# Performance work log

Measured on AMD Instinct MI355X. Metric: run time of the kernel, lower is better.

## Reference

```python
import jax, jax.numpy as jnp
import numpy as np

B, C, W, H = 2, 64, 96, 96
C8 = C // 8


def setup_inputs() -> dict:
    key = jax.random.key(0)
    ks = jax.random.split(key, 8)
    return {
        "x": jax.random.normal(ks[0], (B, C, W, H), dtype=jnp.float32),
        "Wq": jax.random.normal(ks[1], (C8, C), dtype=jnp.float32) * 0.05,
        "bq": jax.random.normal(ks[2], (C8,), dtype=jnp.float32) * 0.05,
        "Wk": jax.random.normal(ks[3], (C8, C), dtype=jnp.float32) * 0.05,
        "bk": jax.random.normal(ks[4], (C8,), dtype=jnp.float32) * 0.05,
        "Wv": jax.random.normal(ks[5], (C, C), dtype=jnp.float32) * 0.05,
        "bv": jax.random.normal(ks[6], (C,), dtype=jnp.float32) * 0.05,
        "gamma": jax.random.normal(ks[7], (1,), dtype=jnp.float32),
    }


def reference(x, Wq, bq, Wk, bk, Wv, bv, gamma):
    b, c, w, h = x.shape
    n = w * h
    xf = x.reshape(b, c, n)  # [B, C, N]
    # 1x1 convs are channel-mixing matmuls over flattened spatial dim
    q = jnp.einsum('oc,bcn->bno', Wq, xf) + bq          # [B, N, C//8] (proj_query, permuted)
    k = jnp.einsum('oc,bcn->bon', Wk, xf) + bk[:, None]  # [B, C//8, N] (proj_key)
    energy = jnp.einsum('bno,bom->bnm', q, k)            # [B, N, N]
    # torch softmax over dim=1 (the query index), NOT the usual dim=-1
    attn = jax.nn.softmax(energy, axis=1)                # [B, N, N]
    v = jnp.einsum('oc,bcn->bon', Wv, xf) + bv[:, None]  # [B, C, N]
    # bmm(V, attn.permute(0,2,1)): out[b,c,m] = sum_n V[b,c,n] * attn[b,m,n]
    out = jnp.einsum('bcn,bmn->bcm', v, attn).reshape(b, c, w, h)
    return gamma * out + x
```

## Files before the change

kernel.cpp:

```cpp
#include <hip/hip_runtime.h>
#include <math.h>

#define NN 9216
#define LOG2E 1.4426950408889634f

typedef __attribute__((ext_vector_type(8))) __bf16 bf16x8;
typedef __attribute__((ext_vector_type(16))) float f32x16;
typedef __attribute__((ext_vector_type(4))) unsigned int u32x4;

#define MFMA32(a,b,c) __builtin_amdgcn_mfma_f32_32x32x16_bf16(a,b,c,0,0,0)

#if __has_builtin(__builtin_amdgcn_exp2f)
#define EXP2(x) __builtin_amdgcn_exp2f(x)
#else
#define EXP2(x) exp2f(x)
#endif

__device__ __forceinline__ bf16x8 zero8() {
    bf16x8 z;
    #pragma unroll
    for (int i = 0; i < 8; i++) z[i] = (__bf16)0.0f;
    return z;
}

__device__ __forceinline__ unsigned int pk2(float a, float b) {
    unsigned short ua = __builtin_bit_cast(unsigned short, (__bf16)a);
    unsigned short ub = __builtin_bit_cast(unsigned short, (__bf16)b);
    return (unsigned int)ua | ((unsigned int)ub << 16);
}

__device__ __forceinline__ void plane_swap(unsigned int &a, unsigned int &b) {
    asm("v_permlane32_swap_b32 %0, %1" : "+v"(a), "+v"(b));
}

__device__ __forceinline__ void cp16(void* lds, const void* g) {
    __builtin_amdgcn_global_load_lds(
        (const __attribute__((address_space(1))) unsigned int*)g,
        (__attribute__((address_space(3))) unsigned int*)lds, 16, 0, 0);
}

#define OFF_QB 0
#define OFF_KB 294912
#define OFF_VB 589824
#define OFF_DP 2949120
#define OFF_PARTS 2949120
#define WS_NEED 21823488ULL

__global__ __launch_bounds__(256) void qkv_kernel(
    const float* __restrict__ x,
    const float* __restrict__ Wq, const float* __restrict__ bq,
    const float* __restrict__ Wk, const float* __restrict__ bk,
    const float* __restrict__ Wv, const float* __restrict__ bv,
    __bf16* __restrict__ QB, __bf16* __restrict__ KB, __bf16* __restrict__ VB)
{
    __shared__ float wvs[1024], wqs[512], wks[512], bvs[16], bqs[8], bks[8];
    int tid = threadIdx.x;
    int z = blockIdx.z, b = blockIdx.y;
    for (int i = tid; i < 1024; i += 256) wvs[i] = Wv[z*1024 + i];
    if (z == 0)
        for (int i = tid; i < 512; i += 256) { wqs[i] = Wq[i]; wks[i] = Wk[i]; }
    if (tid < 16) bvs[tid] = bv[z*16 + tid];
    if (tid < 8)  { bqs[tid] = bq[tid]; bks[tid] = bk[tid]; }
    __syncthreads();

    int n = blockIdx.x * 256 + tid;

    float xc[64];
    #pragma unroll
    for (int c = 0; c < 64; c++) xc[c] = x[((size_t)(b*64 + c))*NN + n];

    float v[16];
    #pragma unroll
    for (int o = 0; o < 16; o++) v[o] = bvs[o];
    #pragma unroll
    for (int c = 0; c < 64; c++) {
        float xv = xc[c];
        #pragma unroll
        for (int o = 0; o < 16; o++) v[o] = fmaf(wvs[o*64+c], xv, v[o]);
    }
    #pragma unroll
    for (int o = 0; o < 16; o++)
        VB[((size_t)(b*64 + z*16 + o))*NN + n] = (__bf16)v[o];

    if (z == 0) {
        float q[8], k[8];
        #pragma unroll
        for (int o = 0; o < 8; o++) { q[o] = bqs[o]; k[o] = bks[o]; }
        #pragma unroll
        for (int c = 0; c < 64; c++) {
            float xv = xc[c];
            #pragma unroll
            for (int o = 0; o < 8; o++) {
                q[o] = fmaf(wqs[o*64+c], xv, q[o]);
                k[o] = fmaf(wks[o*64+c], xv, k[o]);
            }
        }
        bf16x8 qv, kv;
        #pragma unroll
        for (int o = 0; o < 8; o++) {
            qv[o] = (__bf16)(q[o] * LOG2E);
            kv[o] = (__bf16)k[o];
        }
        *(bf16x8*)(QB + ((size_t)b*NN + n)*8) = qv;
        *(bf16x8*)(KB + ((size_t)b*NN + n)*8) = kv;
    }
}

__global__ __launch_bounds__(256) void stats_kernel(
    const __bf16* __restrict__ QB, const __bf16* __restrict__ KB,
    float* __restrict__ Dp)
{
    __shared__ float Dl[4][32];
    int tid = threadIdx.x;
    int lane = tid & 63, w = tid >> 6;
    int l31 = lane & 31, h = lane >> 5;
    int b = blockIdx.y, z = blockIdx.z;
    int n0 = blockIdx.x * 32;

    f32x16 Z16;
    #pragma unroll
    for (int r = 0; r < 16; r++) Z16[r] = 0.0f;

    bf16x8 kf = zero8();
    if (lane < 32)
        kf = *(const bf16x8*)(KB + ((size_t)b*NN + n0 + l31)*8);

    float Dacc[16];
    #pragma unroll
    for (int r = 0; r < 16; r++) Dacc[r] = 0.0f;

    const __bf16* Qb = QB + (size_t)b*NN*8;
    int mbase = z*2304 + w*576;
    for (int it = 0; it < 18; it++) {
        bf16x8 qf = zero8();
        if (lane < 32)
            qf = *(const bf16x8*)(Qb + (size_t)(mbase + it*32 + l31)*8);
        f32x16 e = MFMA32(kf, qf, Z16);
        #pragma unroll
        for (int r = 0; r < 16; r++) Dacc[r] += EXP2(e[r]);
    }
    #pragma unroll
    for (int r = 0; r < 16; r++) {
        #pragma unroll
        for (int mask = 1; mask < 32; mask <<= 1)
            Dacc[r] += __shfl_xor(Dacc[r], mask);
    }
    if (l31 == 0) {
        #pragma unroll
        for (int r = 0; r < 16; r++)
            Dl[w][(r&3) + 8*(r>>2) + 4*h] = Dacc[r];
    }
    __syncthreads();
    if (tid < 32)
        Dp[((size_t)(z*2 + b))*NN + n0 + tid] =
            Dl[0][tid] + Dl[1][tid] + Dl[2][tid] + Dl[3][tid];
}

__global__ __launch_bounds__(256) void fold_kernel(
    const float* __restrict__ Dp, const float* __restrict__ gamma_p,
    __bf16* __restrict__ VB)
{
    __shared__ float Rl[32];
    int tid = threadIdx.x;
    int b = blockIdx.y;
    int n0 = blockIdx.x * 32;
    if (tid < 32) {
        float d = 0.0f;
        #pragma unroll
        for (int zz = 0; zz < 4; zz++)
            d += Dp[((size_t)(zz*2 + b))*NN + n0 + tid];
        Rl[tid] = gamma_p[0] / d;
    }
    __syncthreads();

    int c = tid >> 2, j = tid & 3;
    __bf16* ptr = VB + ((size_t)(b*64 + c))*NN + n0 + j*8;
    bf16x8 vv = *(bf16x8*)ptr;
    #pragma unroll
    for (int i = 0; i < 8; i++)
        vv[i] = (__bf16)((float)vv[i] * Rl[j*8 + i]);
    *(bf16x8*)ptr = vv;
}

__global__ __launch_bounds__(256) void init_kernel(
    const float* __restrict__ x, float* __restrict__ out)
{
    int i = blockIdx.x*256 + threadIdx.x;
    ((float4*)out)[i] = ((const float4*)x)[i];
}

__global__ __launch_bounds__(128) void pv_kernel(
    const __bf16* __restrict__ QB, const __bf16* __restrict__ KB,
    const __bf16* __restrict__ VB, float* __restrict__ out,
    __bf16* __restrict__ parts)
{
    __shared__ __bf16 klin[2][64*8];
    __shared__ __bf16 vbuf[2][64*64];

    int tid = threadIdx.x;
    int lane = tid & 63, w = tid >> 6;
    int l31 = lane & 31, h = lane >> 5;
    int b = blockIdx.y, s = blockIdx.z;
    int mw = blockIdx.x * 64 + w * 32;

    f32x16 Z16;
    #pragma unroll
    for (int r = 0; r < 16; r++) Z16[r] = 0.0f;

    bf16x8 qf = zero8();
    if (lane < 32)
        qf = *(const bf16x8*)(QB + ((size_t)b*NN + mw + l31)*8);

    f32x16 acc[2];
    acc[0] = Z16; acc[1] = Z16;

#define STAGE(bi, stq) do {                                                   \
    int n0_ = s*1152 + (stq)*64;                                              \
    _Pragma("unroll")                                                         \
    for (int i_ = 0; i_ < 4; i_++) {                                          \
        int p2_ = tid + i_*128;                                               \
        int c_ = p2_ >> 3, h7_ = p2_ & 7;                                     \
        int xc_ = h7_ ^ (c_ & 7);                                             \
        cp16((char*)vbuf[bi] + i_*2048 + w*1024,                              \
             VB + ((size_t)(b*64 + c_))*NN + n0_ + xc_*8);                    \
    }                                                                         \
    if (w == 0)                                                               \
        cp16((char*)klin[bi], KB + ((size_t)b*NN + n0_ + lane)*8);            \
} while (0)

    STAGE(0, 0);

    for (int st = 0; st < 18; st++) {
        int bi = st & 1;
        __syncthreads();
        if (st < 17) {
            if (bi == 0) STAGE(1, st+1); else STAGE(0, st+1);
        }
        const __bf16* kl = klin[bi];
        char* vb = (char*)vbuf[bi];

        bf16x8 kfr0 = zero8(), kfr1 = zero8();
        if (lane < 32) {
            kfr0 = *(const bf16x8*)(kl + l31*8);
            kfr1 = *(const bf16x8*)(kl + (32 + l31)*8);
        }
        f32x16 e0 = MFMA32(kfr0, qf, Z16);
        f32x16 e1 = MFMA32(kfr1, qf, Z16);

        bf16x8 pa[2][2];
        #pragma unroll
        for (int nt = 0; nt < 2; nt++) {
            const f32x16& e = nt ? e1 : e0;
            float pf[16];
            #pragma unroll
            for (int r = 0; r < 16; r++) pf[r] = EXP2(e[r]);
            unsigned int u[8];
            #pragma unroll
            for (int q = 0; q < 8; q++) u[q] = pk2(pf[2*q], pf[2*q+1]);
            plane_swap(u[0], u[2]); plane_swap(u[1], u[3]);
            plane_swap(u[4], u[6]); plane_swap(u[5], u[7]);
            u32x4 t0 = {u[0], u[1], u[2], u[3]};
            u32x4 t1 = {u[4], u[5], u[6], u[7]};
            pa[nt][0] = __builtin_bit_cast(bf16x8, t0);
            pa[nt][1] = __builtin_bit_cast(bf16x8, t1);
        }

        __builtin_amdgcn_s_setprio(1);
        #pragma unroll
        for (int nt = 0; nt < 2; nt++)
            #pragma unroll
            for (int ks = 0; ks < 2; ks++)
                #pragma unroll
                for (int ct = 0; ct < 2; ct++) {
                    int c = ct*32 + l31;
                    bf16x8 bfr = *(const bf16x8*)(vb + c*128 +
                        ((nt*64 + ks*32 + h*16) ^ ((c & 7) << 4)));
                    acc[ct] = MFMA32(pa[nt][ks], bfr, acc[ct]);
                }
        __builtin_amdgcn_s_setprio(0);
    }

    if (parts != nullptr) {
        __bf16* pp = parts + ((size_t)(s*2 + b))*64*NN;
        #pragma unroll
        for (int ct = 0; ct < 2; ct++) {
            int c = ct*32 + l31;
            __bf16* row = pp + (size_t)c*NN + mw + 4*h;
            #pragma unroll
            for (int q = 0; q < 4; q++) {
                uint2 v2;
                v2.x = pk2(acc[ct][4*q],   acc[ct][4*q+1]);
                v2.y = pk2(acc[ct][4*q+2], acc[ct][4*q+3]);
                *(uint2*)(row + q*8) = v2;
            }
        }
    } else {
        #pragma unroll
        for (int ct = 0; ct < 2; ct++) {
            int c = ct*32 + l31;
            #pragma unroll
            for (int r = 0; r < 16; r++) {
                int m = mw + (r&3) + 8*(r>>2) + 4*h;
                atomicAdd(out + ((size_t)(b*64 + c))*NN + m, (float)acc[ct][r]);
            }
        }
    }
}

__global__ __launch_bounds__(256) void reduce_kernel(
    const float* __restrict__ x, const __bf16* __restrict__ parts,
    float* __restrict__ out)
{
    size_t f0 = ((size_t)blockIdx.x*256 + threadIdx.x) * 8;
    float o[8];
    float4 a = *(const float4*)(x + f0);
    float4 c = *(const float4*)(x + f0 + 4);
    o[0]=a.x; o[1]=a.y; o[2]=a.z; o[3]=a.w;
    o[4]=c.x; o[5]=c.y; o[6]=c.z; o[7]=c.w;
    #pragma unroll
    for (int sIdx = 0; sIdx < 8; sIdx++) {
        bf16x8 p = *(const bf16x8*)(parts + (size_t)sIdx*(128*NN) + f0);
        #pragma unroll
        for (int j = 0; j < 8; j++) o[j] += (float)p[j];
    }
    float4 r0 = make_float4(o[0],o[1],o[2],o[3]);
    float4 r1 = make_float4(o[4],o[5],o[6],o[7]);
    *(float4*)(out + f0) = r0;
    *(float4*)(out + f0 + 4) = r1;
}

extern "C" void kernel_launch(void* const* d_in, const int* in_sizes, int n_in,
                              void* d_out, int out_size, void* d_ws, size_t ws_size,
                              hipStream_t stream) {
    const float* x     = (const float*)d_in[0];
    const float* Wq    = (const float*)d_in[1];
    const float* bq    = (const float*)d_in[2];
    const float* Wk    = (const float*)d_in[3];
    const float* bk    = (const float*)d_in[4];
    const float* Wv    = (const float*)d_in[5];
    const float* bv    = (const float*)d_in[6];
    const float* gamma = (const float*)d_in[7];
    float* out = (float*)d_out;
    char* ws   = (char*)d_ws;

    __bf16* QB = (__bf16*)(ws + OFF_QB);
    __bf16* KB = (__bf16*)(ws + OFF_KB);
    __bf16* VB = (__bf16*)(ws + OFF_VB);
    float*  Dp = (float*)(ws + OFF_DP);

    qkv_kernel<<<dim3(36, 2, 4), 256, 0, stream>>>(x, Wq, bq, Wk, bk, Wv, bv, QB, KB, VB);
    stats_kernel<<<dim3(288, 2, 4), 256, 0, stream>>>(QB, KB, Dp);
    fold_kernel<<<dim3(288, 2), 256, 0, stream>>>(Dp, gamma, VB);

    if (ws_size >= WS_NEED) {
        __bf16* parts = (__bf16*)(ws + OFF_PARTS);
        pv_kernel<<<dim3(144, 2, 8), 128, 0, stream>>>(QB, KB, VB, out, parts);
        reduce_kernel<<<dim3(576), 256, 0, stream>>>(x, parts, out);
    } else {
        init_kernel<<<dim3(1152), 256, 0, stream>>>(x, out);
        pv_kernel<<<dim3(144, 2, 8), 128, 0, stream>>>(QB, KB, VB, out, nullptr);
    }
}
```

Baseline: 111.3 us.

## Pre-swizzle V into MFMA fragment layout and load it directly to registers

The fold kernel now writes a second copy of the scaled V in a layout that matches the MFMA B-fragment order. pv_kernel can then load V and K fragments straight from global memory into registers with software prefetch, so the LDS staging, swizzle and per-stage __syncthreads are gone. pv blocks grow to 256 threads covering 128 query columns. qkv is also split into 9 z-slices so the V projection runs over more blocks. This adds an extra VF buffer and workspace, and relies on L2 reuse of V across blocks in place of shared memory.

```diff
diff --git a/kernel.cpp b/kernel.cpp
--- a/kernel.cpp
+++ b/kernel.cpp
@@ -33,18 +33,13 @@
     asm("v_permlane32_swap_b32 %0, %1" : "+v"(a), "+v"(b));
 }
 
-__device__ __forceinline__ void cp16(void* lds, const void* g) {
-    __builtin_amdgcn_global_load_lds(
-        (const __attribute__((address_space(1))) unsigned int*)g,
-        (__attribute__((address_space(3))) unsigned int*)lds, 16, 0, 0);
-}
-
 #define OFF_QB 0
 #define OFF_KB 294912
 #define OFF_VB 589824
-#define OFF_DP 2949120
-#define OFF_PARTS 2949120
-#define WS_NEED 21823488ULL
+#define OFF_VF 2949120
+#define OFF_DP 5308416
+#define OFF_PARTS 5308416
+#define WS_NEED 24182784ULL
 
 __global__ __launch_bounds__(256) void qkv_kernel(
     const float* __restrict__ x,
@@ -53,14 +48,16 @@
     const float* __restrict__ Wv, const float* __restrict__ bv,
     __bf16* __restrict__ QB, __bf16* __restrict__ KB, __bf16* __restrict__ VB)
 {
-    __shared__ float wvs[1024], wqs[512], wks[512], bvs[16], bqs[8], bks[8];
+    __shared__ float wsh[1024], bsh[16];
     int tid = threadIdx.x;
     int z = blockIdx.z, b = blockIdx.y;
-    for (int i = tid; i < 1024; i += 256) wvs[i] = Wv[z*1024 + i];
-    if (z == 0)
-        for (int i = tid; i < 512; i += 256) { wqs[i] = Wq[i]; wks[i] = Wk[i]; }
-    if (tid < 16) bvs[tid] = bv[z*16 + tid];
-    if (tid < 8)  { bqs[tid] = bq[tid]; bks[tid] = bk[tid]; }
+    if (z == 0) {
+        for (int i = tid; i < 512; i += 256) { wsh[i] = Wq[i]; wsh[512+i] = Wk[i]; }
+        if (tid < 8)  { bsh[tid] = bq[tid]; bsh[8+tid] = bk[tid]; }
+    } else {
+        for (int i = tid; i < 512; i += 256) wsh[i] = Wv[(z-1)*512 + i];
+        if (tid < 8)  bsh[tid] = bv[(z-1)*8 + tid];
+    }
     __syncthreads();
 
     int n = blockIdx.x * 256 + tid;
@@ -68,31 +65,18 @@
     float xc[64];
     #pragma unroll
     for (int c = 0; c < 64; c++) xc[c] = x[((size_t)(b*64 + c))*NN + n];
-
-    float v[16];
-    #pragma unroll
-    for (int o = 0; o < 16; o++) v[o] = bvs[o];
-    #pragma unroll
-    for (int c = 0; c < 64; c++) {
-        float xv = xc[c];
-        #pragma unroll
-        for (int o = 0; o < 16; o++) v[o] = fmaf(wvs[o*64+c], xv, v[o]);
-    }
-    #pragma unroll
-    for (int o = 0; o < 16; o++)
-        VB[((size_t)(b*64 + z*16 + o))*NN + n] = (__bf16)v[o];
 
     if (z == 0) {
         float q[8], k[8];
         #pragma unroll
-        for (int o = 0; o < 8; o++) { q[o] = bqs[o]; k[o] = bks[o]; }
+        for (int o = 0; o < 8; o++) { q[o] = bsh[o]; k[o] = bsh[8+o]; }
         #pragma unroll
         for (int c = 0; c < 64; c++) {
             float xv = xc[c];
             #pragma unroll
             for (int o = 0; o < 8; o++) {
-                q[o] = fmaf(wqs[o*64+c], xv, q[o]);
-                k[o] = fmaf(wks[o*64+c], xv, k[o]);
+                q[o] = fmaf(wsh[o*64+c], xv, q[o]);
+                k[o] = fmaf(wsh[512+o*64+c], xv, k[o]);
             }
         }
         bf16x8 qv, kv;
@@ -103,6 +87,19 @@
         }
         *(bf16x8*)(QB + ((size_t)b*NN + n)*8) = qv;
         *(bf16x8*)(KB + ((size_t)b*NN + n)*8) = kv;
+    } else {
+        float v[8];
+        #pragma unroll
+        for (int o = 0; o < 8; o++) v[o] = bsh[o];
+        #pragma unroll
+        for (int c = 0; c < 64; c++) {
+            float xv = xc[c];
+            #pragma unroll
+            for (int o = 0; o < 8; o++) v[o] = fmaf(wsh[o*64+c], xv, v[o]);
+        }
+        #pragma unroll
+        for (int o = 0; o < 8; o++)
+            VB[((size_t)(b*64 + (z-1)*8 + o))*NN + n] = (__bf16)v[o];
     }
 }
 
@@ -156,15 +153,15 @@
             Dl[0][tid] + Dl[1][tid] + Dl[2][tid] + Dl[3][tid];
 }
 
-__global__ __launch_bounds__(256) void fold_kernel(
+__global__ __launch_bounds__(256) void foldvf_kernel(
     const float* __restrict__ Dp, const float* __restrict__ gamma_p,
-    __bf16* __restrict__ VB)
-{
-    __shared__ float Rl[32];
+    const __bf16* __restrict__ VB, __bf16* __restrict__ VF)
+{
+    __shared__ float Rl[64];
     int tid = threadIdx.x;
-    int b = blockIdx.y;
-    int n0 = blockIdx.x * 32;
-    if (tid < 32) {
+    int b = blockIdx.y, tg = blockIdx.x;
+    int n0 = tg * 64;
+    if (tid < 64) {
         float d = 0.0f;
         #pragma unroll
         for (int zz = 0; zz < 4; zz++)
@@ -173,13 +170,19 @@
     }
     __syncthreads();
 
-    int c = tid >> 2, j = tid & 3;
-    __bf16* ptr = VB + ((size_t)(b*64 + c))*NN + n0 + j*8;
-    bf16x8 vv = *(bf16x8*)ptr;
-    #pragma unroll
-    for (int i = 0; i < 8; i++)
-        vv[i] = (__bf16)((float)vv[i] * Rl[j*8 + i]);
-    *(bf16x8*)ptr = vv;
+    #pragma unroll
+    for (int i = 0; i < 2; i++) {
+        int p = tid + i*256;
+        int chunk = p >> 6, lane = p & 63;
+        int c  = (chunk & 1)*32 + (lane & 31);
+        int nl = ((chunk >> 2) & 1)*32 + ((chunk >> 1) & 1)*16 + (lane >> 5)*8;
+        bf16x8 v = *(const bf16x8*)(VB + ((size_t)(b*64 + c))*NN + n0 + nl);
+        bf16x8 ov;
+        #pragma unroll
+        for (int j = 0; j < 8; j++)
+            ov[j] = (__bf16)((float)v[j] * Rl[nl + j]);
+        *(bf16x8*)(VF + (((size_t)(b*144 + tg))*8 + chunk)*512 + lane*8) = ov;
+    }
 }
 
 __global__ __launch_bounds__(256) void init_kernel(
@@ -189,19 +192,16 @@
     ((float4*)out)[i] = ((const float4*)x)[i];
 }
 
-__global__ __launch_bounds__(128) void pv_kernel(
+__global__ __launch_bounds__(256) void pv_kernel(
     const __bf16* __restrict__ QB, const __bf16* __restrict__ KB,
-    const __bf16* __restrict__ VB, float* __restrict__ out,
+    const __bf16* __restrict__ VF, float* __restrict__ out,
     __bf16* __restrict__ parts)
 {
-    __shared__ __bf16 klin[2][64*8];
-    __shared__ __bf16 vbuf[2][64*64];
-
     int tid = threadIdx.x;
     int lane = tid & 63, w = tid >> 6;
     int l31 = lane & 31, h = lane >> 5;
     int b = blockIdx.y, s = blockIdx.z;
-    int mw = blockIdx.x * 64 + w * 32;
+    int mw = blockIdx.x * 128 + w * 32;
 
     f32x16 Z16;
     #pragma unroll
@@ -214,38 +214,34 @@
     f32x16 acc[2];
     acc[0] = Z16; acc[1] = Z16;
 
-#define STAGE(bi, stq) do {                                                   \
-    int n0_ = s*1152 + (stq)*64;                                              \
-    _Pragma("unroll")                                                         \
-    for (int i_ = 0; i_ < 4; i_++) {                                          \
-        int p2_ = tid + i_*128;                                               \
-        int c_ = p2_ >> 3, h7_ = p2_ & 7;                                     \
-        int xc_ = h7_ ^ (c_ & 7);                                             \
-        cp16((char*)vbuf[bi] + i_*2048 + w*1024,                              \
-             VB + ((size_t)(b*64 + c_))*NN + n0_ + xc_*8);                    \
-    }                                                                         \
-    if (w == 0)                                                               \
-        cp16((char*)klin[bi], KB + ((size_t)b*NN + n0_ + lane)*8);            \
-} while (0)
-
-    STAGE(0, 0);
-
-    for (int st = 0; st < 18; st++) {
-        int bi = st & 1;
-        __syncthreads();
-        if (st < 17) {
-            if (bi == 0) STAGE(1, st+1); else STAGE(0, st+1);
-        }
-        const __bf16* kl = klin[bi];
-        char* vb = (char*)vbuf[bi];
-
-        bf16x8 kfr0 = zero8(), kfr1 = zero8();
-        if (lane < 32) {
-            kfr0 = *(const bf16x8*)(kl + l31*8);
-            kfr1 = *(const bf16x8*)(kl + (32 + l31)*8);
-        }
-        f32x16 e0 = MFMA32(kfr0, qf, Z16);
-        f32x16 e1 = MFMA32(kfr1, qf, Z16);
+    const __bf16* kbase = KB + ((size_t)b*NN + s*1152)*8;
+    const __bf16* vbase = VF + ((size_t)(b*144 + s*18))*8*512;
+
+    bf16x8 kc0 = zero8(), kc1 = zero8(), kn0 = zero8(), kn1 = zero8();
+    if (lane < 32) {
+        kc0 = *(const bf16x8*)(kbase + l31*8);
+        kc1 = *(const bf16x8*)(kbase + (32 + l31)*8);
+    }
+    bf16x8 vf0, vf1, vf2, vf3, vf4, vf5, vf6, vf7;
+    {
+        const __bf16* vp = vbase + lane*8;
+        vf0 = *(const bf16x8*)(vp + 0*512); vf1 = *(const bf16x8*)(vp + 1*512);
+        vf2 = *(const bf16x8*)(vp + 2*512); vf3 = *(const bf16x8*)(vp + 3*512);
+        vf4 = *(const bf16x8*)(vp + 4*512); vf5 = *(const bf16x8*)(vp + 5*512);
+        vf6 = *(const bf16x8*)(vp + 6*512); vf7 = *(const bf16x8*)(vp + 7*512);
+    }
+
+    for (int t = 0; t < 18; t++) {
+        f32x16 e0 = MFMA32(kc0, qf, Z16);
+        f32x16 e1 = MFMA32(kc1, qf, Z16);
+
+        if (t < 17) {
+            const __bf16* knp = kbase + (t+1)*512;
+            if (lane < 32) {
+                kn0 = *(const bf16x8*)(knp + l31*8);
+                kn1 = *(const bf16x8*)(knp + (32 + l31)*8);
+            }
+        }
 
         bf16x8 pa[2][2];
         #pragma unroll
@@ -266,18 +262,24 @@
         }
 
         __builtin_amdgcn_s_setprio(1);
-        #pragma unroll
-        for (int nt = 0; nt < 2; nt++)
-            #pragma unroll
-            for (int ks = 0; ks < 2; ks++)
-                #pragma unroll
-                for (int ct = 0; ct < 2; ct++) {
-                    int c = ct*32 + l31;
-                    bf16x8 bfr = *(const bf16x8*)(vb + c*128 +
-                        ((nt*64 + ks*32 + h*16) ^ ((c & 7) << 4)));
-                    acc[ct] = MFMA32(pa[nt][ks], bfr, acc[ct]);
-                }
+        acc[0] = MFMA32(pa[0][0], vf0, acc[0]);
+        acc[1] = MFMA32(pa[0][0], vf1, acc[1]);
+        acc[0] = MFMA32(pa[0][1], vf2, acc[0]);
+        acc[1] = MFMA32(pa[0][1], vf3, acc[1]);
+        acc[0] = MFMA32(pa[1][0], vf4, acc[0]);
+        acc[1] = MFMA32(pa[1][0], vf5, acc[1]);
+        acc[0] = MFMA32(pa[1][1], vf6, acc[0]);
+        acc[1] = MFMA32(pa[1][1], vf7, acc[1]);
         __builtin_amdgcn_s_setprio(0);
+
+        if (t < 17) {
+            const __bf16* vp = vbase + (t+1)*4096 + lane*8;
+            vf0 = *(const bf16x8*)(vp + 0*512); vf1 = *(const bf16x8*)(vp + 1*512);
+            vf2 = *(const bf16x8*)(vp + 2*512); vf3 = *(const bf16x8*)(vp + 3*512);
+            vf4 = *(const bf16x8*)(vp + 4*512); vf5 = *(const bf16x8*)(vp + 5*512);
+            vf6 = *(const bf16x8*)(vp + 6*512); vf7 = *(const bf16x8*)(vp + 7*512);
+        }
+        kc0 = kn0; kc1 = kn1;
     }
 
     if (parts != nullptr) {
@@ -346,18 +348,19 @@
     __bf16* QB = (__bf16*)(ws + OFF_QB);
     __bf16* KB = (__bf16*)(ws + OFF_KB);
     __bf16* VB = (__bf16*)(ws + OFF_VB);
+    __bf16* VF = (__bf16*)(ws + OFF_VF);
     float*  Dp = (float*)(ws + OFF_DP);
 
-    qkv_kernel<<<dim3(36, 2, 4), 256, 0, stream>>>(x, Wq, bq, Wk, bk, Wv, bv, QB, KB, VB);
+    qkv_kernel<<<dim3(36, 2, 9), 256, 0, stream>>>(x, Wq, bq, Wk, bk, Wv, bv, QB, KB, VB);
     stats_kernel<<<dim3(288, 2, 4), 256, 0, stream>>>(QB, KB, Dp);
-    fold_kernel<<<dim3(288, 2), 256, 0, stream>>>(Dp, gamma, VB);
+    foldvf_kernel<<<dim3(144, 2), 256, 0, stream>>>(Dp, gamma, VB, VF);
 
     if (ws_size >= WS_NEED) {
         __bf16* parts = (__bf16*)(ws + OFF_PARTS);
-        pv_kernel<<<dim3(144, 2, 8), 128, 0, stream>>>(QB, KB, VB, out, parts);
+        pv_kernel<<<dim3(72, 2, 8), 256, 0, stream>>>(QB, KB, VF, out, parts);
         reduce_kernel<<<dim3(576), 256, 0, stream>>>(x, parts, out);
     } else {
         init_kernel<<<dim3(1152), 256, 0, stream>>>(x, out);
-        pv_kernel<<<dim3(144, 2, 8), 128, 0, stream>>>(QB, KB, VB, out, nullptr);
-    }
-}
+        pv_kernel<<<dim3(72, 2, 8), 256, 0, stream>>>(QB, KB, VF, out, nullptr);
+    }
+}
```

Result: faster. 102.3 us (-8.1%).
